# Kernel optimization log

Measured on AMD Instinct MI355X. Metric: run time of the kernel, lower is better.

The kernel has to match this reference:

```python
import jax, jax.numpy as jnp
import numpy as np

# Model config (matches init_kwargs)
HIDDEN = 2048
N_HEADS = 32
N_KV_HEADS = 8
HEAD_DIM = 64
BS = 8  # block_size_x = block_size_y = block_size_z


def setup_inputs() -> dict:
    key = jax.random.key(0)
    ks = jax.random.split(key, 5)
    B, X, Y, Z = 2, 16, 16, 16
    L = X * Y * Z  # 4096
    s = 1.0 / np.sqrt(HIDDEN)
    return {
        "hidden_states": jax.random.normal(ks[0], (B, L, HIDDEN), jnp.float32),
        "Wq": jax.random.normal(ks[1], (N_HEADS * HEAD_DIM, HIDDEN), jnp.float32) * s,
        "Wk": jax.random.normal(ks[2], (N_KV_HEADS * HEAD_DIM, HIDDEN), jnp.float32) * s,
        "Wv": jax.random.normal(ks[3], (N_KV_HEADS * HEAD_DIM, HIDDEN), jnp.float32) * s,
        "Wo": jax.random.normal(ks[4], (HIDDEN, N_HEADS * HEAD_DIM), jnp.float32) * s,
        "x_dim": 16,
        "y_dim": 16,
        "z_dim": 16,
    }


def _to_blocks(t, B, x_dim, y_dim, z_dim, H):
    # t: [B, L, H*D] with L interpreted as (x, y, z) row-major grid.
    # einops: 'b (bnx bsx bny bsy bnz bsz) (h d) -> (b bnx bny bnz) (bsx bsy bsz) h d'
    bnx, bny, bnz = x_dim // BS, y_dim // BS, z_dim // BS
    t = t.reshape(B, bnx, BS, bny, BS, bnz, BS, H, HEAD_DIM)
    t = t.transpose(0, 1, 3, 5, 2, 4, 6, 7, 8)  # [B,bnx,bny,bnz,bsx,bsy,bsz,H,D]
    return t.reshape(B * bnx * bny * bnz, BS * BS * BS, H, HEAD_DIM)


def _from_blocks(o, B, x_dim, y_dim, z_dim):
    bnx, bny, bnz = x_dim // BS, y_dim // BS, z_dim // BS
    o = o.reshape(B, bnx, bny, bnz, BS, BS, BS, N_HEADS, HEAD_DIM)
    o = o.transpose(0, 1, 4, 2, 5, 3, 6, 7, 8)  # back to (bnx bsx bny bsy bnz bsz)
    return o.reshape(B, x_dim * y_dim * z_dim, N_HEADS * HEAD_DIM)


def reference(hidden_states, Wq, Wk, Wv, Wo, x_dim, y_dim, z_dim):
    B, L, _ = hidden_states.shape
    q = _to_blocks(hidden_states @ Wq.T, B, x_dim, y_dim, z_dim, N_HEADS)     # [NB,T,H,D]
    k = _to_blocks(hidden_states @ Wk.T, B, x_dim, y_dim, z_dim, N_KV_HEADS)  # [NB,T,Hk,D]
    v = _to_blocks(hidden_states @ Wv.T, B, x_dim, y_dim, z_dim, N_KV_HEADS)
    # GQA: repeat kv heads across groups (flash_attn handles this internally)
    g = N_HEADS // N_KV_HEADS
    k = jnp.repeat(k, g, axis=2)
    v = jnp.repeat(v, g, axis=2)
    scale = HEAD_DIM ** -0.5
    # non-causal full attention within each 3D block
    scores = jnp.einsum('bthd,bshd->bhts', q, k) * scale  # [NB,H,T,T]
    p = jax.nn.softmax(scores, axis=-1)
    o = jnp.einsum('bhts,bshd->bthd', p, v)               # [NB,T,H,D]
    o = _from_blocks(o, B, x_dim, y_dim, z_dim)           # [B,L,H*D]
    return o @ Wo.T
```

## Files before the change

### kernel.cpp

```cpp
#include <hip/hip_runtime.h>

typedef _Float16 f16;
typedef _Float16 f16x4 __attribute__((ext_vector_type(4)));
typedef _Float16 f16x8 __attribute__((ext_vector_type(8)));
typedef float f32x4 __attribute__((ext_vector_type(4)));
typedef unsigned int u32;
typedef u32 u32x4 __attribute__((ext_vector_type(4)));

__device__ __forceinline__ void gld_lds16(const void* g, void* l) {
  __builtin_amdgcn_global_load_lds(
      (const __attribute__((address_space(1))) void*)g,
      (__attribute__((address_space(3))) void*)l, 16, 0, 0);
}

__device__ __forceinline__ u32 pkrtz(float a, float b) {
  return __builtin_bit_cast(u32, __builtin_amdgcn_cvt_pkrtz(a, b));
}

#define XSWZ(row) (((row) & 7) << 4)

__global__ __launch_bounds__(256) void cast5_k(
    const float4* s0, const float4* s1, const float4* s2, const float4* s3,
    const float4* s4, f16x4* d0, f16x4* d1, f16x4* d2, f16x4* d3, f16x4* d4,
    int e0, int e1, int e2, int e3, int e4) {
  int i = blockIdx.x * blockDim.x + threadIdx.x;
  int stride = gridDim.x * blockDim.x;
  for (; i < e4; i += stride) {
    const float4* s = s0; f16x4* d = d0; int base = 0;
    if (i >= e0) { s = s1; d = d1; base = e0; }
    if (i >= e1) { s = s2; d = d2; base = e1; }
    if (i >= e2) { s = s3; d = d3; base = e2; }
    if (i >= e3) { s = s4; d = d4; base = e3; }
    float4 v = s[i - base];
    f16x4 o;
    o.x = (f16)v.x; o.y = (f16)v.y; o.z = (f16)v.z; o.w = (f16)v.w;
    d[i - base] = o;
  }
}

template <typename OutT>
__global__ __launch_bounds__(256, 2) void gemm_bt(
    const f16* __restrict__ A, const f16* __restrict__ B, OutT* __restrict__ C,
    int M, int N, int K, float oscale) {
  __shared__ __align__(16) f16 Al[128 * 64];
  __shared__ __align__(16) f16 Bl[128 * 64];
  const int tid = threadIdx.x;
  const int lane = tid & 63;
  const int wave = tid >> 6;
  const int bm = blockIdx.x, bn = blockIdx.y;
  const int wm = wave >> 1, wn = wave & 1;
  f32x4 acc[4][4] = {};

  const size_t ldb = (size_t)K * 2;
  const char* Ab = (const char*)A + (size_t)bm * 128 * ldb;
  const char* Bb = (const char*)B + (size_t)bn * 128 * ldb;

  const int kTiles = K >> 6;
  for (int kt = 0; kt < kTiles; ++kt) {
    const size_t kOff = (size_t)kt << 7;
    __syncthreads();
#pragma unroll
    for (int i = 0; i < 4; ++i) {
      int c = i * 256 + tid;
      int row = c >> 3;
      int colb = ((c & 7) << 4) ^ XSWZ(row);
      gld_lds16(Ab + (size_t)row * ldb + kOff + colb,
                (char*)Al + (i * 256 + wave * 64) * 16);
      gld_lds16(Bb + (size_t)row * ldb + kOff + colb,
                (char*)Bl + (i * 256 + wave * 64) * 16);
    }
    __syncthreads();
#pragma unroll
    for (int kk = 0; kk < 2; ++kk) {
      const int kb = kk * 64 + ((lane >> 4) << 4);
      f16x8 af[4], bf[4];
#pragma unroll
      for (int mf = 0; mf < 4; ++mf) {
        int row = wm * 64 + mf * 16 + (lane & 15);
        af[mf] = *(const f16x8*)((const char*)Al + (row << 7) + (kb ^ XSWZ(row)));
      }
#pragma unroll
      for (int nf = 0; nf < 4; ++nf) {
        int row = wn * 64 + nf * 16 + (lane & 15);
        bf[nf] = *(const f16x8*)((const char*)Bl + (row << 7) + (kb ^ XSWZ(row)));
      }
#pragma unroll
      for (int mf = 0; mf < 4; ++mf)
#pragma unroll
        for (int nf = 0; nf < 4; ++nf)
          acc[mf][nf] = __builtin_amdgcn_mfma_f32_16x16x32_f16(af[mf], bf[nf], acc[mf][nf], 0, 0, 0);
    }
  }
  const int r0 = ((lane >> 4) << 2);
  const int cl = lane & 15;
#pragma unroll
  for (int mf = 0; mf < 4; ++mf)
#pragma unroll
    for (int r = 0; r < 4; ++r) {
      size_t row = (size_t)bm * 128 + wm * 64 + mf * 16 + r0 + r;
#pragma unroll
      for (int nf = 0; nf < 4; ++nf) {
        int col = bn * 128 + wn * 64 + nf * 16 + cl;
        C[row * N + col] = (OutT)(acc[mf][nf][r] * oscale);
      }
    }
}

__device__ __forceinline__ int tok_row(int nb, int t) {
  int b = nb >> 3;
  int x = (((nb >> 2) & 1) << 3) | (t >> 6);
  int y = (((nb >> 1) & 1) << 3) | ((t >> 3) & 7);
  int z = ((nb & 1) << 3) | (t & 7);
  return (b << 12) | (x << 8) | (y << 4) | z;
}

__global__ __launch_bounds__(256) void attn3d(
    const f16* __restrict__ Q, const f16* __restrict__ KV, f16* __restrict__ O) {
  __shared__ __align__(16) f16 Ql[128 * 64];
  __shared__ __align__(16) f16 Kl[64 * 64];
  __shared__ __align__(16) f16 Vt[64 * 64];
  const int tid = threadIdx.x;
  const int lane = tid & 63;
  const int wave = tid >> 6;
  const int fid = blockIdx.x;
  const int orig = (fid & 7) * 256 + (fid >> 3);
  const int qt = orig & 3, h = (orig >> 2) & 31, nb = orig >> 7;
  const int hk = h >> 2;
  const int l15 = lane & 15;
  const int g = lane >> 4;
  const size_t ldkv = 2048;

  const int pos2 = (((lane & 3) | (((lane >> 4) & 1) << 2) |
                     (((lane >> 2) & 3) << 3) | ((lane >> 5) << 5))) * 2;

#pragma unroll
  for (int i = 0; i < 4; ++i) {
    int c = i * 256 + tid;
    int row = c >> 3;
    int colb = ((c & 7) << 4) ^ XSWZ(row);
    gld_lds16((const char*)Q + (size_t)tok_row(nb, qt * 128 + row) * 4096 + h * 128 + colb,
              (char*)Ql + (i * 256 + wave * 64) * 16);
  }
  __syncthreads();
  f16x8 bq[2][2];
#pragma unroll
  for (int qf = 0; qf < 2; ++qf)
#pragma unroll
    for (int kk = 0; kk < 2; ++kk) {
      int row = wave * 32 + qf * 16 + l15;
      int kb = kk * 64 + (g << 4);
      bq[qf][kk] = *(const f16x8*)((const char*)Ql + (row << 7) + (kb ^ XSWZ(row)));
    }

  f32x4 o[2][4] = {};
  float lacc[2] = {0.f, 0.f};

  for (int kt = 0; kt < 8; ++kt) {
    f16x8 vch[2];
#pragma unroll
    for (int it = 0; it < 2; ++it) {
      int idx = it * 256 + tid;
      int kv = idx & 63, dc = idx >> 6;
      vch[it] = *(const f16x8*)((const char*)KV +
          (size_t)tok_row(nb, kt * 64 + kv) * ldkv + 1024 + hk * 128 + dc * 16);
    }
    __syncthreads();
#pragma unroll
    for (int i = 0; i < 2; ++i) {
      int c = i * 256 + tid;
      int row = c >> 3;
      int colb = ((c & 7) << 4) ^ XSWZ(row);
      gld_lds16((const char*)KV + (size_t)tok_row(nb, kt * 64 + row) * ldkv + hk * 128 + colb,
                (char*)Kl + (i * 256 + wave * 64) * 16);
    }
#pragma unroll
    for (int it = 0; it < 2; ++it) {
      const int dbase = (it * 4 + wave) * 8;
#pragma unroll
      for (int j = 0; j < 8; ++j)
        *(f16*)((char*)Vt + ((dbase + j) << 7) + (pos2 ^ (j << 4))) = vch[it][j];
    }
    __syncthreads();
    f32x4 s[2][4] = {};
    __builtin_amdgcn_s_setprio(1);
#pragma unroll
    for (int kk = 0; kk < 2; ++kk) {
      const int kb = kk * 64 + (g << 4);
      f16x8 ka[4];
#pragma unroll
      for (int nf = 0; nf < 4; ++nf) {
        int krow = nf * 16 + l15;
        ka[nf] = *(const f16x8*)((const char*)Kl + (krow << 7) + (kb ^ XSWZ(krow)));
      }
#pragma unroll
      for (int qf = 0; qf < 2; ++qf)
#pragma unroll
        for (int nf = 0; nf < 4; ++nf)
          s[qf][nf] = __builtin_amdgcn_mfma_f32_16x16x32_f16(ka[nf], bq[qf][kk], s[qf][nf], 0, 0, 0);
    }
    __builtin_amdgcn_s_setprio(0);
#pragma unroll
    for (int qf = 0; qf < 2; ++qf) {
      float ls = 0.f;
#pragma unroll
      for (int nf = 0; nf < 4; ++nf)
#pragma unroll
        for (int r = 0; r < 4; ++r) {
          float p = __builtin_amdgcn_exp2f(s[qf][nf][r]);
          s[qf][nf][r] = p;
          ls += p;
        }
      lacc[qf] += ls;
    }
    __builtin_amdgcn_s_setprio(1);
#pragma unroll
    for (int kh = 0; kh < 2; ++kh) {
      f16x8 va[4];
      const int cb = kh * 64 + g * 16;
#pragma unroll
      for (int df = 0; df < 4; ++df) {
        int d = df * 16 + l15;
        va[df] = *(const f16x8*)((const char*)Vt + (d << 7) + (cb ^ XSWZ(d)));
      }
#pragma unroll
      for (int qf = 0; qf < 2; ++qf) {
        u32x4 pw = {pkrtz(s[qf][2 * kh][0], s[qf][2 * kh][1]),
                    pkrtz(s[qf][2 * kh][2], s[qf][2 * kh][3]),
                    pkrtz(s[qf][2 * kh + 1][0], s[qf][2 * kh + 1][1]),
                    pkrtz(s[qf][2 * kh + 1][2], s[qf][2 * kh + 1][3])};
        f16x8 pf = __builtin_bit_cast(f16x8, pw);
#pragma unroll
        for (int df = 0; df < 4; ++df)
          o[qf][df] = __builtin_amdgcn_mfma_f32_16x16x32_f16(va[df], pf, o[qf][df], 0, 0, 0);
      }
    }
    __builtin_amdgcn_s_setprio(0);
  }
#pragma unroll
  for (int qf = 0; qf < 2; ++qf) {
    float l = lacc[qf];
    l += __shfl_xor(l, 16);
    l += __shfl_xor(l, 32);
    float inv = 1.f / l;
    int t = qt * 128 + wave * 32 + qf * 16 + l15;
    char* dst = (char*)O + (size_t)tok_row(nb, t) * 4096 + h * 128;
#pragma unroll
    for (int df = 0; df < 4; ++df) {
      f16x4 o4;
#pragma unroll
      for (int r = 0; r < 4; ++r) o4[r] = (f16)(o[qf][df][r] * inv);
      *(f16x4*)(dst + df * 32 + g * 8) = o4;
    }
  }
}

extern "C" void kernel_launch(void* const* d_in, const int* in_sizes, int n_in,
                              void* d_out, int out_size, void* d_ws, size_t ws_size,
                              hipStream_t stream) {
  (void)in_sizes; (void)n_in; (void)out_size; (void)ws_size;
  const float* hs = (const float*)d_in[0];
  const float* Wq = (const float*)d_in[1];
  const float* Wk = (const float*)d_in[2];
  const float* Wv = (const float*)d_in[3];
  const float* Wo = (const float*)d_in[4];
  float* out = (float*)d_out;
  char* ws = (char*)d_ws;

  f16* hid16 = (f16*)(ws + 0);
  f16* Wq16  = (f16*)(ws + 33554432);
  f16* Wk16  = (f16*)(ws + 41943040);
  f16* Wv16  = (f16*)(ws + 44040192);
  f16* Wo16  = (f16*)(ws + 46137344);
  f16* Q16   = (f16*)(ws + 54525952);
  f16* KV16  = (f16*)(ws + 88080384);

  cast5_k<<<2048, 256, 0, stream>>>(
      (const float4*)hs, (const float4*)Wq, (const float4*)Wk,
      (const float4*)Wv, (const float4*)Wo,
      (f16x4*)hid16, (f16x4*)Wq16, (f16x4*)Wk16, (f16x4*)Wv16, (f16x4*)Wo16,
      4194304, 5242880, 5505024, 5767168, 6815744);

  gemm_bt<f16><<<dim3(64, 16), 256, 0, stream>>>(hid16, Wq16, Q16, 8192, 2048, 2048,
                                                 0.18033688011112042f);
  gemm_bt<f16><<<dim3(64, 8), 256, 0, stream>>>(hid16, Wk16, KV16, 8192, 1024, 2048, 1.0f);

  attn3d<<<2048, 256, 0, stream>>>(Q16, KV16, hid16);

  gemm_bt<float><<<dim3(64, 16), 256, 0, stream>>>(hid16, Wo16, out, 8192, 2048, 2048, 1.0f);
}
```

Baseline: 274.7 us.

## Add 256x256-tile 8-wave pipelined GEMM for Q and output projections

Adds a new GEMM kernel with 256x256 output tiles, 8 waves per block and 128KB of LDS. It double-buffers K-halves with direct global-to-LDS loads, and loads are interleaved between MFMA phases under barriers and raised wave priority. The Q projection and the output projection now use it, while the KV projection keeps the old 128x128 kernel. The larger tiles raise data reuse per LDS load and hide global latency, at the cost of only 256 blocks, which risks low occupancy and a partial wave at the end on 256 CUs.

```diff
diff --git a/kernel.cpp b/kernel.cpp
--- a/kernel.cpp
+++ b/kernel.cpp
@@ -6,6 +6,10 @@
 typedef float f32x4 __attribute__((ext_vector_type(4)));
 typedef unsigned int u32;
 typedef u32 u32x4 __attribute__((ext_vector_type(4)));
+
+__device__ __forceinline__ f32x4 mfma16(f16x8 a, f16x8 b, f32x4 c) {
+  return __builtin_amdgcn_mfma_f32_16x16x32_f16(a, b, c, 0, 0, 0);
+}
 
 __device__ __forceinline__ void gld_lds16(const void* g, void* l) {
   __builtin_amdgcn_global_load_lds(
@@ -88,7 +92,7 @@
       for (int mf = 0; mf < 4; ++mf)
 #pragma unroll
         for (int nf = 0; nf < 4; ++nf)
-          acc[mf][nf] = __builtin_amdgcn_mfma_f32_16x16x32_f16(af[mf], bf[nf], acc[mf][nf], 0, 0, 0);
+          acc[mf][nf] = mfma16(af[mf], bf[nf], acc[mf][nf]);
     }
   }
   const int r0 = ((lane >> 4) << 2);
@@ -102,6 +106,131 @@
       for (int nf = 0; nf < 4; ++nf) {
         int col = bn * 128 + wn * 64 + nf * 16 + cl;
         C[row * N + col] = (OutT)(acc[mf][nf][r] * oscale);
+      }
+    }
+}
+
+template <typename OutT>
+__global__ __launch_bounds__(512, 2) void gemm_bt8(
+    const f16* __restrict__ A, const f16* __restrict__ B, OutT* __restrict__ C,
+    int M, int N, int K, float oscale) {
+  __shared__ __align__(16) char lds[131072];
+  const int tid = threadIdx.x;
+  const int lane = tid & 63;
+  const int wave = tid >> 6;
+  const int wm = wave >> 2, wn = wave & 3;
+  const int l15 = lane & 15, g = lane >> 4;
+  const int bm = blockIdx.x >> 3, bn = blockIdx.x & 7;
+
+  const size_t ldb = (size_t)K * 2;
+  const int r0 = tid >> 2, r1 = 128 + (tid >> 2);
+  const int chx = (((tid & 3) ^ (r0 & 3)) << 4);
+  const char* As0 = (const char*)A + (size_t)(bm * 256 + r0) * ldb + chx;
+  const char* As1 = (const char*)A + (size_t)(bm * 256 + r1) * ldb + chx;
+  const char* Bs0 = (const char*)B + (size_t)(bn * 256 + r0) * ldb + chx;
+  const char* Bs1 = (const char*)B + (size_t)(bn * 256 + r1) * ldb + chx;
+
+  auto stA = [&](int buf, int t, int kh) {
+    char* dst = (char*)lds + (buf * 2 + kh) * 16384 + wave * 1024;
+    size_t ko = (size_t)t * 128 + (size_t)kh * 64;
+    gld_lds16(As0 + ko, dst);
+    gld_lds16(As1 + ko, dst + 8192);
+  };
+  auto stB = [&](int buf, int t, int kh) {
+    char* dst = (char*)lds + 65536 + (buf * 2 + kh) * 16384 + wave * 1024;
+    size_t ko = (size_t)t * 128 + (size_t)kh * 64;
+    gld_lds16(Bs0 + ko, dst);
+    gld_lds16(Bs1 + ko, dst + 8192);
+  };
+
+  int aoff[8], boff[4];
+  const int rsw = (g ^ (l15 & 3)) << 4;
+#pragma unroll
+  for (int mf = 0; mf < 8; ++mf)
+    aoff[mf] = (wm * 128 + mf * 16 + l15) * 64 + rsw;
+#pragma unroll
+  for (int nf = 0; nf < 4; ++nf)
+    boff[nf] = (wn * 64 + nf * 16 + l15) * 64 + rsw;
+
+  f32x4 acc[8][4] = {};
+
+  stA(0, 0, 0); stB(0, 0, 0); stA(0, 0, 1); stB(0, 0, 1);
+  stA(1, 1, 0); stB(1, 1, 0); stA(1, 1, 1);
+  asm volatile("s_waitcnt vmcnt(6)" ::: "memory");
+  __builtin_amdgcn_s_barrier();
+
+  const int nkt = K >> 6;
+  for (int T = 0; T < nkt; ++T) {
+    const int cur = T & 1;
+    const char* A0 = (const char*)lds + (cur * 2 + 0) * 16384;
+    const char* A1 = (const char*)lds + (cur * 2 + 1) * 16384;
+    const char* B0r = (const char*)lds + 65536 + (cur * 2 + 0) * 16384;
+    const char* B1r = (const char*)lds + 65536 + (cur * 2 + 1) * 16384;
+    f16x8 a[8], b0, b1;
+#pragma unroll
+    for (int mf = 0; mf < 8; ++mf) a[mf] = *(const f16x8*)(A0 + aoff[mf]);
+    b0 = *(const f16x8*)(B0r + boff[0]);
+    b1 = *(const f16x8*)(B0r + boff[1]);
+    if (T + 1 < nkt) stB(cur ^ 1, T + 1, 1);
+    __builtin_amdgcn_s_barrier();
+    __builtin_amdgcn_s_setprio(1);
+#pragma unroll
+    for (int mf = 0; mf < 8; ++mf) {
+      acc[mf][0] = mfma16(a[mf], b0, acc[mf][0]);
+      acc[mf][1] = mfma16(a[mf], b1, acc[mf][1]);
+    }
+    __builtin_amdgcn_s_setprio(0);
+    __builtin_amdgcn_s_barrier();
+    b0 = *(const f16x8*)(B0r + boff[2]);
+    b1 = *(const f16x8*)(B0r + boff[3]);
+    if (T + 2 < nkt) stA(cur, T + 2, 0);
+    __builtin_amdgcn_s_barrier();
+    __builtin_amdgcn_s_setprio(1);
+#pragma unroll
+    for (int mf = 0; mf < 8; ++mf) {
+      acc[mf][2] = mfma16(a[mf], b0, acc[mf][2]);
+      acc[mf][3] = mfma16(a[mf], b1, acc[mf][3]);
+    }
+    __builtin_amdgcn_s_setprio(0);
+    __builtin_amdgcn_s_barrier();
+#pragma unroll
+    for (int mf = 0; mf < 8; ++mf) a[mf] = *(const f16x8*)(A1 + aoff[mf]);
+    b0 = *(const f16x8*)(B1r + boff[0]);
+    b1 = *(const f16x8*)(B1r + boff[1]);
+    if (T + 2 < nkt) stB(cur, T + 2, 0);
+    __builtin_amdgcn_s_barrier();
+    __builtin_amdgcn_s_setprio(1);
+#pragma unroll
+    for (int mf = 0; mf < 8; ++mf) {
+      acc[mf][0] = mfma16(a[mf], b0, acc[mf][0]);
+      acc[mf][1] = mfma16(a[mf], b1, acc[mf][1]);
+    }
+    __builtin_amdgcn_s_setprio(0);
+    __builtin_amdgcn_s_barrier();
+    b0 = *(const f16x8*)(B1r + boff[2]);
+    b1 = *(const f16x8*)(B1r + boff[3]);
+    if (T + 2 < nkt) stA(cur, T + 2, 1);
+    if (T < nkt - 2) asm volatile("s_waitcnt vmcnt(6)" ::: "memory");
+    else             asm volatile("s_waitcnt vmcnt(0)" ::: "memory");
+    __builtin_amdgcn_s_barrier();
+    __builtin_amdgcn_s_setprio(1);
+#pragma unroll
+    for (int mf = 0; mf < 8; ++mf) {
+      acc[mf][2] = mfma16(a[mf], b0, acc[mf][2]);
+      acc[mf][3] = mfma16(a[mf], b1, acc[mf][3]);
+    }
+    __builtin_amdgcn_s_setprio(0);
+    __builtin_amdgcn_s_barrier();
+  }
+#pragma unroll
+  for (int mf = 0; mf < 8; ++mf)
+#pragma unroll
+    for (int r = 0; r < 4; ++r) {
+      size_t row = (size_t)bm * 256 + wm * 128 + mf * 16 + g * 4 + r;
+#pragma unroll
+      for (int nf = 0; nf < 4; ++nf) {
+        int col = bn * 256 + wn * 64 + nf * 16 + l15;
+        C[row * (size_t)N + col] = (OutT)(acc[mf][nf][r] * oscale);
       }
     }
 }
@@ -196,7 +325,7 @@
       for (int qf = 0; qf < 2; ++qf)
 #pragma unroll
         for (int nf = 0; nf < 4; ++nf)
-          s[qf][nf] = __builtin_amdgcn_mfma_f32_16x16x32_f16(ka[nf], bq[qf][kk], s[qf][nf], 0, 0, 0);
+          s[qf][nf] = mfma16(ka[nf], bq[qf][kk], s[qf][nf]);
     }
     __builtin_amdgcn_s_setprio(0);
 #pragma unroll
@@ -231,7 +360,7 @@
         f16x8 pf = __builtin_bit_cast(f16x8, pw);
 #pragma unroll
         for (int df = 0; df < 4; ++df)
-          o[qf][df] = __builtin_amdgcn_mfma_f32_16x16x32_f16(va[df], pf, o[qf][df], 0, 0, 0);
+          o[qf][df] = mfma16(va[df], pf, o[qf][df]);
       }
     }
     __builtin_amdgcn_s_setprio(0);
@@ -280,11 +409,11 @@
       (f16x4*)hid16, (f16x4*)Wq16, (f16x4*)Wk16, (f16x4*)Wv16, (f16x4*)Wo16,
       4194304, 5242880, 5505024, 5767168, 6815744);
 
-  gemm_bt<f16><<<dim3(64, 16), 256, 0, stream>>>(hid16, Wq16, Q16, 8192, 2048, 2048,
-                                                 0.18033688011112042f);
+  gemm_bt8<f16><<<256, 512, 0, stream>>>(hid16, Wq16, Q16, 8192, 2048, 2048,
+                                         0.18033688011112042f);
   gemm_bt<f16><<<dim3(64, 8), 256, 0, stream>>>(hid16, Wk16, KV16, 8192, 1024, 2048, 1.0f);
 
   attn3d<<<2048, 256, 0, stream>>>(Q16, KV16, hid16);
 
-  gemm_bt<float><<<dim3(64, 16), 256, 0, stream>>>(hid16, Wo16, out, 8192, 2048, 2048, 1.0f);
-}
+  gemm_bt8<float><<<256, 512, 0, stream>>>(hid16, Wo16, out, 8192, 2048, 2048, 1.0f);
+}
```

Measured after the change: 280.4 us. +2.1%, slower.

## Replace GEMM with 256x256-tile 8-wave pipelined kernel and fuse QKV launches

Applied to the files above, without the earlier changes.

The 128x128 GEMM becomes a 512-thread kernel that computes 256x256 tiles. It double-buffers K-tiles in 128KB of LDS, issues async global-to-LDS loads interleaved with MFMA clusters, and coordinates them with explicit vmcnt waits and barriers. The Q and KV projections merge into one launch, with blocks where bn>=8 writing to the KV buffer, and a swizzled block index improves L2 reuse. The goal is higher MFMA utilisation and less launch and load overhead. The costs are one block per CU, a hardcoded N of 2048, and a schedule that depends on matrix sizes dividing the tile evenly.

```diff
diff --git a/kernel.cpp b/kernel.cpp
--- a/kernel.cpp
+++ b/kernel.cpp
@@ -6,6 +6,10 @@
 typedef float f32x4 __attribute__((ext_vector_type(4)));
 typedef unsigned int u32;
 typedef u32 u32x4 __attribute__((ext_vector_type(4)));
+
+__device__ __forceinline__ f32x4 mfma16(f16x8 a, f16x8 b, f32x4 c) {
+  return __builtin_amdgcn_mfma_f32_16x16x32_f16(a, b, c, 0, 0, 0);
+}
 
 __device__ __forceinline__ void gld_lds16(const void* g, void* l) {
   __builtin_amdgcn_global_load_lds(
@@ -39,71 +43,147 @@
 }
 
 template <typename OutT>
-__global__ __launch_bounds__(256, 2) void gemm_bt(
+__global__ __launch_bounds__(512, 1) void gemm_bt8(
     const f16* __restrict__ A, const f16* __restrict__ B, OutT* __restrict__ C,
-    int M, int N, int K, float oscale) {
-  __shared__ __align__(16) f16 Al[128 * 64];
-  __shared__ __align__(16) f16 Bl[128 * 64];
+    f16* __restrict__ Ckv, int K, float oscale) {
+  __shared__ __align__(16) char lds[131072];
   const int tid = threadIdx.x;
   const int lane = tid & 63;
   const int wave = tid >> 6;
-  const int bm = blockIdx.x, bn = blockIdx.y;
-  const int wm = wave >> 1, wn = wave & 1;
-  f32x4 acc[4][4] = {};
+  const int wm = wave >> 2, wn = wave & 3;
+  const int l15 = lane & 15, g = lane >> 4;
+  const int bid = blockIdx.x;
+  const int bm = (bid & 7) * 4 + ((bid >> 3) & 3);
+  const int bn = bid >> 5;
 
   const size_t ldb = (size_t)K * 2;
-  const char* Ab = (const char*)A + (size_t)bm * 128 * ldb;
-  const char* Bb = (const char*)B + (size_t)bn * 128 * ldb;
-
-  const int kTiles = K >> 6;
-  for (int kt = 0; kt < kTiles; ++kt) {
-    const size_t kOff = (size_t)kt << 7;
-    __syncthreads();
-#pragma unroll
-    for (int i = 0; i < 4; ++i) {
-      int c = i * 256 + tid;
-      int row = c >> 3;
-      int colb = ((c & 7) << 4) ^ XSWZ(row);
-      gld_lds16(Ab + (size_t)row * ldb + kOff + colb,
-                (char*)Al + (i * 256 + wave * 64) * 16);
-      gld_lds16(Bb + (size_t)row * ldb + kOff + colb,
-                (char*)Bl + (i * 256 + wave * 64) * 16);
-    }
-    __syncthreads();
-#pragma unroll
-    for (int kk = 0; kk < 2; ++kk) {
-      const int kb = kk * 64 + ((lane >> 4) << 4);
-      f16x8 af[4], bf[4];
-#pragma unroll
-      for (int mf = 0; mf < 4; ++mf) {
-        int row = wm * 64 + mf * 16 + (lane & 15);
-        af[mf] = *(const f16x8*)((const char*)Al + (row << 7) + (kb ^ XSWZ(row)));
-      }
-#pragma unroll
-      for (int nf = 0; nf < 4; ++nf) {
-        int row = wn * 64 + nf * 16 + (lane & 15);
-        bf[nf] = *(const f16x8*)((const char*)Bl + (row << 7) + (kb ^ XSWZ(row)));
-      }
-#pragma unroll
-      for (int mf = 0; mf < 4; ++mf)
-#pragma unroll
-        for (int nf = 0; nf < 4; ++nf)
-          acc[mf][nf] = __builtin_amdgcn_mfma_f32_16x16x32_f16(af[mf], bf[nf], acc[mf][nf], 0, 0, 0);
-    }
-  }
-  const int r0 = ((lane >> 4) << 2);
-  const int cl = lane & 15;
-#pragma unroll
-  for (int mf = 0; mf < 4; ++mf)
-#pragma unroll
-    for (int r = 0; r < 4; ++r) {
-      size_t row = (size_t)bm * 128 + wm * 64 + mf * 16 + r0 + r;
-#pragma unroll
-      for (int nf = 0; nf < 4; ++nf) {
-        int col = bn * 128 + wn * 64 + nf * 16 + cl;
-        C[row * N + col] = (OutT)(acc[mf][nf][r] * oscale);
-      }
-    }
+  const int r0 = tid >> 2, r1 = 128 + (tid >> 2);
+  const int chx = (((tid & 3) ^ ((tid >> 3) & 3)) << 4);
+  const char* As0 = (const char*)A + (size_t)(bm * 256 + r0) * ldb + chx;
+  const char* As1 = (const char*)A + (size_t)(bm * 256 + r1) * ldb + chx;
+  const char* Bs0 = (const char*)B + (size_t)(bn * 256 + r0) * ldb + chx;
+  const char* Bs1 = (const char*)B + (size_t)(bn * 256 + r1) * ldb + chx;
+
+  auto stA = [&](int buf, int t, int kh) {
+    char* dst = (char*)lds + (buf * 2 + kh) * 16384 + wave * 1024;
+    size_t ko = (size_t)t * 128 + (size_t)kh * 64;
+    gld_lds16(As0 + ko, dst);
+    gld_lds16(As1 + ko, dst + 8192);
+  };
+  auto stB = [&](int buf, int t, int kh) {
+    char* dst = (char*)lds + 65536 + (buf * 2 + kh) * 16384 + wave * 1024;
+    size_t ko = (size_t)t * 128 + (size_t)kh * 64;
+    gld_lds16(Bs0 + ko, dst);
+    gld_lds16(Bs1 + ko, dst + 8192);
+  };
+
+  int aoff[8], boff[4];
+  const int rsw = (g ^ ((l15 >> 1) & 3)) << 4;
+#pragma unroll
+  for (int mf = 0; mf < 8; ++mf)
+    aoff[mf] = (wm * 128 + mf * 16 + l15) * 64 + rsw;
+#pragma unroll
+  for (int nf = 0; nf < 4; ++nf)
+    boff[nf] = (wn * 64 + nf * 16 + l15) * 64 + rsw;
+
+  f32x4 acc[8][4] = {};
+  f16x8 aA[8], aB[8], bE0, bE1, bO0, bO1;
+
+  stA(0, 0, 0); stB(0, 0, 0); stA(0, 0, 1); stB(0, 0, 1);
+  stA(1, 1, 0); stB(1, 1, 0); stA(1, 1, 1);
+  asm volatile("s_waitcnt vmcnt(6)" ::: "memory");
+#pragma unroll
+  for (int mf = 0; mf < 8; ++mf)
+    aA[mf] = *(const f16x8*)(lds + aoff[mf]);
+  bE0 = *(const f16x8*)(lds + 65536 + boff[0]);
+  bE1 = *(const f16x8*)(lds + 65536 + boff[1]);
+  __builtin_amdgcn_s_barrier();
+
+  const int nkt = K >> 6;
+
+#define MFMA_CLUST(aset, bx, by, n0, n1)                 \
+  __builtin_amdgcn_s_setprio(1);                         \
+  _Pragma("unroll") for (int mf = 0; mf < 8; ++mf) {     \
+    acc[mf][n0] = mfma16(aset[mf], bx, acc[mf][n0]);     \
+    acc[mf][n1] = mfma16(aset[mf], by, acc[mf][n1]);     \
+  }                                                      \
+  __builtin_amdgcn_s_setprio(0);
+
+#define TILE(CUR)                                                           \
+  do {                                                                      \
+    const char* A1c = lds + ((CUR)*2 + 1) * 16384;                          \
+    const char* B0c = lds + 65536 + ((CUR)*2 + 0) * 16384;                  \
+    const char* B1c = lds + 65536 + ((CUR)*2 + 1) * 16384;                  \
+    const char* A0n = lds + (((CUR) ^ 1) * 2 + 0) * 16384;                  \
+    const char* B0n = lds + 65536 + (((CUR) ^ 1) * 2 + 0) * 16384;          \
+                                    \
+    if (T + 1 < nkt) stB((CUR) ^ 1, T + 1, 1);                              \
+    bO0 = *(const f16x8*)(B0c + boff[2]);                                   \
+    bO1 = *(const f16x8*)(B0c + boff[3]);                                   \
+    __builtin_amdgcn_s_barrier();                                           \
+    MFMA_CLUST(aA, bE0, bE1, 0, 1)                                          \
+    __builtin_amdgcn_s_barrier();                                           \
+                            \
+    if (T + 2 < nkt) stA((CUR), T + 2, 0);                                  \
+    _Pragma("unroll") for (int mf = 0; mf < 8; ++mf)                        \
+        aB[mf] = *(const f16x8*)(A1c + aoff[mf]);                           \
+    bE0 = *(const f16x8*)(B1c + boff[0]);                                   \
+    bE1 = *(const f16x8*)(B1c + boff[1]);                                   \
+    __builtin_amdgcn_s_barrier();                                           \
+    MFMA_CLUST(aA, bO0, bO1, 2, 3)                                          \
+    __builtin_amdgcn_s_barrier();                                           \
+                                    \
+    if (T + 2 < nkt) stB((CUR), T + 2, 0);                                  \
+    bO0 = *(const f16x8*)(B1c + boff[2]);                                   \
+    bO1 = *(const f16x8*)(B1c + boff[3]);                                   \
+    __builtin_amdgcn_s_barrier();                                           \
+    MFMA_CLUST(aB, bE0, bE1, 0, 1)                                          \
+    __builtin_amdgcn_s_barrier();                                           \
+           \
+    if (T + 2 < nkt) stA((CUR), T + 2, 1);                                  \
+    if (T < nkt - 2) asm volatile("s_waitcnt vmcnt(6)" ::: "memory");       \
+    else             asm volatile("s_waitcnt vmcnt(0)" ::: "memory");       \
+    _Pragma("unroll") for (int mf = 0; mf < 8; ++mf)                        \
+        aA[mf] = *(const f16x8*)(A0n + aoff[mf]);                           \
+    bE0 = *(const f16x8*)(B0n + boff[0]);                                   \
+    bE1 = *(const f16x8*)(B0n + boff[1]);                                   \
+    __builtin_amdgcn_s_barrier();                                           \
+    MFMA_CLUST(aB, bO0, bO1, 2, 3)                                          \
+    __builtin_amdgcn_s_barrier();                                           \
+  } while (0)
+
+  for (int T2 = 0; T2 < nkt; T2 += 2) {
+    { int T = T2;     TILE(0); }
+    { int T = T2 + 1; TILE(1); }
+  }
+#undef TILE
+#undef MFMA_CLUST
+
+  if (Ckv && bn >= 8) {
+#pragma unroll
+    for (int mf = 0; mf < 8; ++mf)
+#pragma unroll
+      for (int r = 0; r < 4; ++r) {
+        size_t row = (size_t)bm * 256 + wm * 128 + mf * 16 + g * 4 + r;
+#pragma unroll
+        for (int nf = 0; nf < 4; ++nf) {
+          int col = (bn - 8) * 256 + wn * 64 + nf * 16 + l15;
+          Ckv[row * 1024 + col] = (f16)acc[mf][nf][r];
+        }
+      }
+  } else {
+#pragma unroll
+    for (int mf = 0; mf < 8; ++mf)
+#pragma unroll
+      for (int r = 0; r < 4; ++r) {
+        size_t row = (size_t)bm * 256 + wm * 128 + mf * 16 + g * 4 + r;
+#pragma unroll
+        for (int nf = 0; nf < 4; ++nf) {
+          int col = bn * 256 + wn * 64 + nf * 16 + l15;
+          C[row * 2048 + col] = (OutT)(acc[mf][nf][r] * oscale);
+        }
+      }
+  }
 }
 
 __device__ __forceinline__ int tok_row(int nb, int t) {
@@ -196,7 +276,7 @@
       for (int qf = 0; qf < 2; ++qf)
 #pragma unroll
         for (int nf = 0; nf < 4; ++nf)
-          s[qf][nf] = __builtin_amdgcn_mfma_f32_16x16x32_f16(ka[nf], bq[qf][kk], s[qf][nf], 0, 0, 0);
+          s[qf][nf] = mfma16(ka[nf], bq[qf][kk], s[qf][nf]);
     }
     __builtin_amdgcn_s_setprio(0);
 #pragma unroll
@@ -231,7 +311,7 @@
         f16x8 pf = __builtin_bit_cast(f16x8, pw);
 #pragma unroll
         for (int df = 0; df < 4; ++df)
-          o[qf][df] = __builtin_amdgcn_mfma_f32_16x16x32_f16(va[df], pf, o[qf][df], 0, 0, 0);
+          o[qf][df] = mfma16(va[df], pf, o[qf][df]);
       }
     }
     __builtin_amdgcn_s_setprio(0);
@@ -280,11 +360,10 @@
       (f16x4*)hid16, (f16x4*)Wq16, (f16x4*)Wk16, (f16x4*)Wv16, (f16x4*)Wo16,
       4194304, 5242880, 5505024, 5767168, 6815744);
 
-  gemm_bt<f16><<<dim3(64, 16), 256, 0, stream>>>(hid16, Wq16, Q16, 8192, 2048, 2048,
-                                                 0.18033688011112042f);
-  gemm_bt<f16><<<dim3(64, 8), 256, 0, stream>>>(hid16, Wk16, KV16, 8192, 1024, 2048, 1.0f);
+  gemm_bt8<f16><<<384, 512, 0, stream>>>(hid16, Wq16, Q16, KV16, 2048,
+                                         0.18033688011112042f);
 
   attn3d<<<2048, 256, 0, stream>>>(Q16, KV16, hid16);
 
-  gemm_bt<float><<<dim3(64, 16), 256, 0, stream>>>(hid16, Wo16, out, 8192, 2048, 2048, 1.0f);
-}
+  gemm_bt8<float><<<256, 512, 0, stream>>>(hid16, Wo16, out, nullptr, 2048, 1.0f);
+}
```

After: 379.0 us. +38.0%, slower.
